# Kernel tuning notes

Hardware: AMD Instinct MI355X
Metric: run time of the kernel (lower is better)

The kernel has to match this reference:

```python
import jax, jax.numpy as jnp
import numpy as np

B, T, E, H, K, V = 64, 256, 300, 500, 64, 32000  # batch, seq, embed, hidden/dir, tags, vocab
PAD, EOS, SOS = 0, 1, 2
NEG = -10000.0


def setup_inputs() -> dict:
    key = jax.random.key(0)
    ks = jax.random.split(key, 20)
    rn = lambda k, shape, s=0.05: jax.random.normal(k, shape, jnp.float32) * s
    inp = {}
    inp["x"] = jax.random.randint(ks[0], (B, T), 3, V)   # all > 0 -> mask all ones (no padding)
    inp["y0"] = jax.random.randint(ks[1], (B, T), 3, K)  # gold tags, avoid PAD/EOS/SOS
    inp["embed"] = rn(ks[2], (V, E), 0.1)
    dims = [E, 2 * H]  # layer-0 input = embed, layer-1 input = concat(bi-dir hidden)
    i = 3
    for l in (0, 1):
        for d in ("f", "b"):
            inp[f"Wih{l}{d}"] = rn(ks[i], (4 * H, dims[l])); i += 1
            inp[f"Whh{l}{d}"] = rn(ks[i], (4 * H, H)); i += 1
            inp[f"b{l}{d}"] = rn(ks[i], (4 * H,)); i += 1
    inp["Wout"] = rn(ks[i], (K, 2 * H))
    inp["bout"] = rn(ks[i + 1], (K,))
    tr = jax.random.normal(ks[i + 2], (K, K), jnp.float32)
    tr = (tr.at[SOS, :].set(NEG).at[:, EOS].set(NEG).at[:, PAD].set(NEG)
            .at[PAD, :].set(NEG).at[PAD, EOS].set(0.0).at[PAD, PAD].set(0.0))
    inp["trans"] = tr  # trans[next, prev]
    return inp


def _lstm_dir(xs, Wih, Whh, b, reverse):
    """xs: [T,B,D] -> [T,B,H]; PyTorch gate order i,f,g,o."""
    if reverse:
        xs = xs[::-1]
    z0 = jnp.zeros((xs.shape[1], Whh.shape[1]), xs.dtype)

    def step(carry, xt):
        h, c = carry
        z = xt @ Wih.T + h @ Whh.T + b
        i_, f_, g_, o_ = jnp.split(z, 4, axis=-1)
        c = jax.nn.sigmoid(f_) * c + jax.nn.sigmoid(i_) * jnp.tanh(g_)
        h = jax.nn.sigmoid(o_) * jnp.tanh(c)
        return (h, c), h

    _, hs = jax.lax.scan(step, (z0, z0), xs)
    return hs[::-1] if reverse else hs


def reference(x, y0, embed, Wih0f, Whh0f, b0f, Wih0b, Whh0b, b0b,
              Wih1f, Whh1f, b1f, Wih1b, Whh1b, b1b, Wout, bout, trans):
    xs = embed[x].transpose(1, 0, 2)  # [T,B,E]
    h0 = jnp.concatenate([_lstm_dir(xs, Wih0f, Whh0f, b0f, False),
                          _lstm_dir(xs, Wih0b, Whh0b, b0b, True)], axis=-1)
    h1 = jnp.concatenate([_lstm_dir(h0, Wih1f, Whh1f, b1f, False),
                          _lstm_dir(h0, Wih1b, Whh1b, b1b, True)], axis=-1)
    emit = h1 @ Wout.T + bout                  # [T,B,K]
    mask = (x > 0).astype(emit.dtype).T        # [T,B]
    emit = emit * mask[..., None]              # y = y * mask

    # CRF partition (forward algorithm): new[b,j] = LSE_i(score[b,i] + trans[j,i]) + emit[t,b,j]
    init = jnp.full((B, K), NEG, emit.dtype).at[:, SOS].set(0.0)

    def step(score, em):
        e_t, m_t = em
        new = jax.nn.logsumexp(score[:, None, :] + trans[None, :, :], axis=-1) + e_t
        return jnp.where(m_t[:, None] > 0, new, score), None

    final, _ = jax.lax.scan(step, init, (emit, mask))
    Z = jax.nn.logsumexp(final, axis=-1)       # [B]

    # gold path score
    tags = jnp.concatenate([jnp.full((B, 1), SOS, y0.dtype), y0], axis=1)  # [B,T+1]
    e = jnp.take_along_axis(emit.transpose(1, 0, 2), tags[:, 1:, None], axis=2)[..., 0]  # [B,T]
    tr = trans[tags[:, 1:], tags[:, :-1]] * mask.T                                       # [B,T]
    gold = (e + tr).sum(axis=1)
    return Z - gold
```

## Files before the change

### kernel.cpp

```cpp
#include <hip/hip_runtime.h>
#include <hip/hip_bf16.h>

typedef short bf16x4 __attribute__((ext_vector_type(4)));
typedef short bf16x8 __attribute__((ext_vector_type(8)));
typedef short bf16x16 __attribute__((ext_vector_type(16)));
typedef float f32x4 __attribute__((ext_vector_type(4)));
typedef __hip_bfloat16 bf16;
typedef unsigned long long ull;

#define NEGV -10000.0f


__device__ __forceinline__ float sigm(float v) { return 1.0f / (1.0f + __expf(-v)); }
__device__ __forceinline__ float tanh_(float v) { float e = __expf(2.0f * v); return 1.0f - 2.0f / (e + 1.0f); }

__device__ __forceinline__ void async_load16(const bf16* g, const char* l) {
  __builtin_amdgcn_global_load_lds((const __attribute__((address_space(1))) void*)g,
                                   (__attribute__((address_space(3))) void*)l, 16, 0, 0);
}


__global__ __launch_bounds__(256) void pack_w0(const float* __restrict__ wf, const float* __restrict__ wb,
                                               bf16* __restrict__ dst) {
  int idx = blockIdx.x * 256 + threadIdx.x;
  int u = idx & 7, lane = (idx >> 3) & 63, rem = idx >> 9;
  int kt = rem % 10, nt = rem / 10;
  int n = (nt << 4) + (lane & 15), k = (kt << 5) + ((lane >> 4) << 3) + u;
  int d = n >> 11, g = (n >> 9) & 3, j = n & 511;
  float v = 0.f;
  if (j < 500 && k < 300) v = (d ? wb : wf)[(g * 500 + j) * 300 + k];
  dst[idx] = __float2bfloat16(v);
}

__global__ __launch_bounds__(256) void pack_whh(const float* __restrict__ w, bf16* __restrict__ dst) {
  int idx = blockIdx.x * 256 + threadIdx.x;
  int u = idx & 7, lane = (idx >> 3) & 63, rem = idx >> 9;
  int kt = rem & 15, nt = rem >> 4;
  int n = (nt << 4) + (lane & 15), k = (kt << 5) + ((lane >> 4) << 3) + u;
  int g = n >> 9, j = n & 511;
  float v = 0.f;
  if (j < 500 && k < 500) v = w[(g * 500 + j) * 500 + k];
  dst[idx] = __float2bfloat16(v);
}

__global__ __launch_bounds__(256) void pack_w1(const float* __restrict__ wf, const float* __restrict__ wb,
                                               bf16* __restrict__ dst) {
  int idx = blockIdx.x * 256 + threadIdx.x;
  int u = idx & 7, lane = (idx >> 3) & 63, rem = idx >> 9;
  int kt = rem & 31, nt = rem >> 5;
  int n = (nt << 4) + (lane & 15), k = (kt << 5) + ((lane >> 4) << 3) + u;
  int d = n >> 11, g = (n >> 9) & 3, j = n & 511;
  int kk = k & 511;
  int ks = (k < 512) ? kk : 500 + kk;
  float v = 0.f;
  if (j < 500 && kk < 500) v = (d ? wb : wf)[(g * 500 + j) * 1000 + ks];
  dst[idx] = __float2bfloat16(v);
}

__global__ __launch_bounds__(256) void pack_wout(const float* __restrict__ w, bf16* __restrict__ dst) {
  int idx = blockIdx.x * 256 + threadIdx.x;
  int u = idx & 7, lane = (idx >> 3) & 63, rem = idx >> 9;
  int kt = rem & 31, nt = rem >> 5;
  int n = (nt << 4) + (lane & 15), k = (kt << 5) + ((lane >> 4) << 3) + u;
  int kk = k & 511;
  int ks = (k < 512) ? kk : 500 + kk;
  float v = 0.f;
  if (kk < 500) v = w[n * 1000 + ks];
  dst[idx] = __float2bfloat16(v);
}

__global__ __launch_bounds__(256) void pack_bias(const float* __restrict__ bf_, const float* __restrict__ bb_,
                                                 float* __restrict__ dst) {
  int idx = blockIdx.x * 256 + threadIdx.x;
  int d = idx >> 11, g = (idx >> 9) & 3, j = idx & 511;
  dst[idx] = (j < 500) ? (d ? bb_ : bf_)[g * 500 + j] : 0.f;
}

__global__ __launch_bounds__(256) void embed_k(const int* __restrict__ x, const float* __restrict__ em,
                                               bf16* __restrict__ xs) {
  int idx = blockIdx.x * 256 + threadIdx.x;
  int e = idx % 320;
  int row = idx / 320;
  int t = row >> 6, b = row & 63;
  float v = 0.f;
  if (e < 300) {
    int xv = x[b * 256 + t];
    v = em[(size_t)xv * 300 + e];
  }
  xs[idx] = __float2bfloat16(v);
}

__global__ __launch_bounds__(256) void gemm_nt(const bf16* __restrict__ A, const bf16* __restrict__ Bf,
                                               bf16* __restrict__ C, int Kdim, int Kt) {
  const int lane = threadIdx.x & 63, wave = threadIdx.x >> 6;
  const int lr = lane & 15, lh = lane >> 4;
  const int mb = blockIdx.x * 64;
  const int ntb = blockIdx.y * 16 + wave * 4;
  f32x4 acc[4][4] = {};
  for (int kt = 0; kt < Kt; ++kt) {
    bf16x8 a[4], b[4];
#pragma unroll
    for (int mt = 0; mt < 4; ++mt)
      a[mt] = *(const bf16x8*)(A + (size_t)(mb + mt * 16 + lr) * Kdim + kt * 32 + lh * 8);
#pragma unroll
    for (int q = 0; q < 4; ++q)
      b[q] = *(const bf16x8*)(Bf + ((size_t)(ntb + q) * Kt + kt) * 512 + lane * 8);
#pragma unroll
    for (int mt = 0; mt < 4; ++mt)
#pragma unroll
      for (int q = 0; q < 4; ++q)
        acc[mt][q] = __builtin_amdgcn_mfma_f32_16x16x32_bf16(a[mt], b[q], acc[mt][q], 0, 0, 0);
  }
  const int t = blockIdx.x;
#pragma unroll
  for (int q = 0; q < 4; ++q) {
    const int colbase = (ntb + q) * 16;
    const int dirq = colbase >> 11, gq = (colbase >> 9) & 3, jbq = (colbase >> 4) & 31;
    unsigned short vals[16];
#pragma unroll
    for (int mt = 0; mt < 4; ++mt)
#pragma unroll
      for (int r = 0; r < 4; ++r) {
        bf16 hb = __float2bfloat16(acc[mt][q][r]);
        vals[mt * 4 + r] = *(unsigned short*)&hb;
      }
    bf16* outp = C + ((((size_t)t * 2 + dirq) * 32 + jbq) * 4 + gq) * 1024 + lane * 16;
    *(bf16x8*)(outp) = *(const bf16x8*)(vals);
    *(bf16x8*)(outp + 8) = *(const bf16x8*)(vals + 8);
  }
}

template <int ROWS>
__global__ __launch_bounds__(256, 1) void lstm_st(const bf16* __restrict__ preP, const bf16* __restrict__ whh,
                                                  const float* __restrict__ bias, bf16* __restrict__ hout,
                                                  unsigned int* __restrict__ flags) {
  constexpr int MT = ROWS / 16;
  constexpr int NPART = 64 / ROWS;
  const int tid = threadIdx.x, lane = tid & 63, wave = tid >> 6;
  const int lr = lane & 15, lh = lane >> 4;
  const int jb = blockIdx.x, dir = blockIdx.y, part = blockIdx.z;
  unsigned int* flg = flags + (dir * NPART + part) * 64;
  unsigned int* myflg = flg + jb;
  __shared__ __align__(64) char hlds[ROWS * 1040];
  __shared__ float xch[4 * ROWS * 17];
  __shared__ float cst[ROWS * 16];
  for (int i = tid; i < ROWS * 16; i += 256) cst[i] = 0.f;
  const float bb = bias[dir * 2048 + wave * 512 + jb * 16 + lr];
  const bf16* wbase = whh + ((size_t)(dir * 128 + wave * 32 + jb) * 16) * 512 + lane * 8;

  bf16x8 wfrag[16];
#pragma unroll
  for (int kt = 0; kt < 16; ++kt) wfrag[kt] = *(const bf16x8*)(wbase + kt * 512);

  unsigned short pf[MT * 4];
  {
    const int t0 = dir ? 255 : 0;
    const bf16* pb = preP + ((((size_t)t0 * 2 + dir) * 32 + jb) * 4 + wave) * 1024 + lane * 16 + part * MT * 4;
    if constexpr (MT == 1) *(bf16x4*)pf = *(const bf16x4*)pb;
    else if constexpr (MT == 2) *(bf16x8*)pf = *(const bf16x8*)pb;
    else *(bf16x16*)pf = *(const bf16x16*)pb;
  }

  for (int s = 0; s < 256; ++s) {
    const int t = dir ? 255 - s : s;
    f32x4 acc[MT] = {};
    if (s > 0) {
      const unsigned int tgt = (unsigned int)s;
      for (;;) {
        unsigned int v = __hip_atomic_load(flg + (lane & 31), __ATOMIC_RELAXED, __HIP_MEMORY_SCOPE_AGENT);
        if (__all((int)(v >= tgt))) break;
      }
      asm volatile("" ::: "memory");
      const int tp = dir ? t + 1 : t - 1;
      const bf16* hp = hout + (size_t)tp * 65536 + dir * 512;
#pragma unroll
      for (int i = 0; i < ROWS / 4; ++i) {
        const int row = i * 4 + wave;
        async_load16(hp + (size_t)(part * ROWS + row) * 1024 + lane * 8, hlds + row * 1040);
      }
      asm volatile("s_waitcnt vmcnt(0)" ::: "memory");
      __syncthreads();
#pragma unroll 4
      for (int kt = 0; kt < 16; ++kt) {
#pragma unroll
        for (int mt = 0; mt < MT; ++mt) {
          const int row = mt * 16 + lr;
          const bf16x8 afr = *(const bf16x8*)(hlds + row * 1040 + kt * 64 + lh * 16);
          acc[mt] = __builtin_amdgcn_mfma_f32_16x16x32_bf16(afr, wfrag[kt], acc[mt], 0, 0, 0);
        }
      }
    }
#pragma unroll
    for (int mt = 0; mt < MT; ++mt)
#pragma unroll
      for (int r = 0; r < 4; ++r) {
        bf16 pv; *(unsigned short*)&pv = pf[mt * 4 + r];
        xch[(wave * ROWS + mt * 16 + lh * 4 + r) * 17 + lr] = acc[mt][r] + bb + __bfloat162float(pv);
      }
    __syncthreads();
    if (tid < ROWS * 8) {
      const int row = tid >> 3, c0 = (tid & 7) * 2;
      unsigned int pk = 0;
#pragma unroll
      for (int i = 0; i < 2; ++i) {
        int col = c0 + i;
        float gi = xch[(0 * ROWS + row) * 17 + col];
        float gf = xch[(1 * ROWS + row) * 17 + col];
        float gg = xch[(2 * ROWS + row) * 17 + col];
        float go = xch[(3 * ROWS + row) * 17 + col];
        float c = cst[row * 16 + col];
        float cn = sigm(gf) * c + sigm(gi) * tanh_(gg);
        cst[row * 16 + col] = cn;
        bf16 hb = __float2bfloat16(sigm(go) * tanh_(cn));
        pk |= (unsigned int)(*(unsigned short*)&hb) << (16 * i);
      }
      unsigned int* hq =
          (unsigned int*)(hout + ((size_t)t * 64 + part * ROWS + row) * 1024 + dir * 512 + jb * 16 + c0);
      __hip_atomic_store(hq, pk, __ATOMIC_RELAXED, __HIP_MEMORY_SCOPE_AGENT);
    }
    asm volatile("s_waitcnt vmcnt(0)" ::: "memory");
    __syncthreads();
    if (tid == 0)
      __hip_atomic_store(myflg, (unsigned int)(s + 1), __ATOMIC_RELAXED, __HIP_MEMORY_SCOPE_AGENT);
    if (s < 255) {
      const int tn = dir ? t - 1 : t + 1;
      const bf16* pb = preP + ((((size_t)tn * 2 + dir) * 32 + jb) * 4 + wave) * 1024 + lane * 16 + part * MT * 4;
      if constexpr (MT == 1) *(bf16x4*)pf = *(const bf16x4*)pb;
      else if constexpr (MT == 2) *(bf16x8*)pf = *(const bf16x8*)pb;
      else *(bf16x16*)pf = *(const bf16x16*)pb;
    }
  }
}

__global__ __launch_bounds__(256) void emit_k(const bf16* __restrict__ h1, const bf16* __restrict__ wo,
                                              const float* __restrict__ bout, const int* __restrict__ x,
                                              float* __restrict__ emit) {
  const int tid = threadIdx.x, lane = tid & 63, wave = tid >> 6;
  const int lr = lane & 15, lh = lane >> 4;
  const int mb = blockIdx.x * 64 + wave * 16;
  f32x4 acc[4] = {};
  for (int kt = 0; kt < 32; ++kt) {
    bf16x8 a = *(const bf16x8*)(h1 + (size_t)(mb + lr) * 1024 + kt * 32 + lh * 8);
#pragma unroll
    for (int q = 0; q < 4; ++q) {
      bf16x8 b = *(const bf16x8*)(wo + ((size_t)(q * 32 + kt) * 64 + lane) * 8);
      acc[q] = __builtin_amdgcn_mfma_f32_16x16x32_bf16(a, b, acc[q], 0, 0, 0);
    }
  }
#pragma unroll
  for (int q = 0; q < 4; ++q)
#pragma unroll
    for (int r = 0; r < 4; ++r) {
      int row = mb + lh * 4 + r;
      int col = q * 16 + lr;
      int tt = row >> 6, bi = row & 63;
      float m = (x[bi * 256 + tt] > 0) ? 1.f : 0.f;
      emit[(size_t)row * 64 + col] = (acc[q][r] + bout[col]) * m;
    }
}

__global__ __launch_bounds__(256) void crf_k(const float* __restrict__ emit, const float* __restrict__ trans,
                                             const int* __restrict__ x, const int* __restrict__ y0,
                                             float* __restrict__ out) {
  const int b = blockIdx.x, tid = threadIdx.x;
  __shared__ float tr[4096];
  __shared__ float sc[2][64];
  __shared__ float pm[4][64], ps[4][64];
  __shared__ float redw[4];
  for (int i = tid; i < 4096; i += 256) tr[i] = trans[i];
  if (tid < 64) sc[0][tid] = (tid == 2) ? 0.f : NEGV;
  __syncthreads();
  {
    const int t = tid;
    const int tag = y0[b * 256 + t];
    const int prev = t ? y0[b * 256 + t - 1] : 2;
    const float m = (x[b * 256 + t] > 0) ? 1.f : 0.f;
    float g = emit[((size_t)t * 64 + b) * 64 + tag] + tr[tag * 64 + prev] * m;
    for (int o = 32; o; o >>= 1) g += __shfl_down(g, o, 64);
    if ((tid & 63) == 0) redw[tid >> 6] = g;
  }
  __syncthreads();
  const float gold = redw[0] + redw[1] + redw[2] + redw[3];
  const int j = tid & 63, kq = tid >> 6;
  int cur = 0;
  for (int t = 0; t < 256; ++t) {
    const float* trj = tr + j * 64 + kq * 16;
    const float* scc = sc[cur] + kq * 16;
    float v[16];
    float mx = -3.0e38f;
#pragma unroll
    for (int k = 0; k < 16; ++k) {
      v[k] = scc[k] + trj[k];
      mx = fmaxf(mx, v[k]);
    }
    float sm = 0.f;
#pragma unroll
    for (int k = 0; k < 16; ++k) sm += __expf(v[k] - mx);
    pm[kq][j] = mx;
    ps[kq][j] = sm;
    __syncthreads();
    if (kq == 0) {
      float M = fmaxf(fmaxf(pm[0][j], pm[1][j]), fmaxf(pm[2][j], pm[3][j]));
      float S = ps[0][j] * __expf(pm[0][j] - M) + ps[1][j] * __expf(pm[1][j] - M) +
                ps[2][j] * __expf(pm[2][j] - M) + ps[3][j] * __expf(pm[3][j] - M);
      float nv = M + __logf(S) + emit[((size_t)t * 64 + b) * 64 + j];
      sc[cur ^ 1][j] = (x[b * 256 + t] > 0) ? nv : sc[cur][j];
    }
    __syncthreads();
    cur ^= 1;
  }
  if (tid < 64) {
    float v2 = sc[cur][tid];
    float M = v2;
    for (int o = 32; o; o >>= 1) M = fmaxf(M, __shfl_xor(M, o, 64));
    float s2 = __expf(v2 - M);
    for (int o = 32; o; o >>= 1) s2 += __shfl_xor(s2, o, 64);
    if (tid == 0) out[b] = M + __logf(s2) - gold;
  }
}

extern "C" void kernel_launch(void* const* d_in, const int* in_sizes, int n_in, void* d_out, int out_size,
                              void* d_ws, size_t ws_size, hipStream_t stream) {
  (void)in_sizes; (void)n_in; (void)out_size; (void)ws_size;
  const int* x = (const int*)d_in[0];
  const int* y0 = (const int*)d_in[1];
  const float* embed = (const float*)d_in[2];
  const float* Wih0f = (const float*)d_in[3];
  const float* Whh0f = (const float*)d_in[4];
  const float* b0f = (const float*)d_in[5];
  const float* Wih0b = (const float*)d_in[6];
  const float* Whh0b = (const float*)d_in[7];
  const float* b0b = (const float*)d_in[8];
  const float* Wih1f = (const float*)d_in[9];
  const float* Whh1f = (const float*)d_in[10];
  const float* b1f = (const float*)d_in[11];
  const float* Wih1b = (const float*)d_in[12];
  const float* Whh1b = (const float*)d_in[13];
  const float* b1b = (const float*)d_in[14];
  const float* Wout = (const float*)d_in[15];
  const float* bout = (const float*)d_in[16];
  const float* trans = (const float*)d_in[17];

  char* p = (char*)d_ws;
  auto take = [&](size_t n) { char* r = p; p += (n + 255) & ~(size_t)255; return r; };
  unsigned int* flags = (unsigned int*)take(2048 * sizeof(unsigned int));
  bf16* xs = (bf16*)take(16384ull * 320 * 2);
  bf16* preP = (bf16*)take(16384ull * 4096 * 2);
  bf16* h0 = (bf16*)take(16384ull * 1024 * 2);
  bf16* h1 = (bf16*)take(16384ull * 1024 * 2);
  float* emitb = (float*)take(16384ull * 64 * 4);
  bf16* W0B = (bf16*)take(4096ull * 320 * 2);
  bf16* W1B = (bf16*)take(4096ull * 1024 * 2);
  bf16* WhhB = (bf16*)take(4ull * 1048576 * 2);
  bf16* WoB = (bf16*)take(64ull * 1024 * 2);
  float* bias0 = (float*)take(4096 * 4);
  float* bias1 = (float*)take(4096 * 4);

  hipMemsetAsync(flags, 0, 2048 * sizeof(unsigned int), stream);
  hipLaunchKernelGGL(pack_w0, dim3(5120), dim3(256), 0, stream, Wih0f, Wih0b, W0B);
  hipLaunchKernelGGL(pack_whh, dim3(4096), dim3(256), 0, stream, Whh0f, WhhB + 0ull * 1048576);
  hipLaunchKernelGGL(pack_whh, dim3(4096), dim3(256), 0, stream, Whh0b, WhhB + 1ull * 1048576);
  hipLaunchKernelGGL(pack_whh, dim3(4096), dim3(256), 0, stream, Whh1f, WhhB + 2ull * 1048576);
  hipLaunchKernelGGL(pack_whh, dim3(4096), dim3(256), 0, stream, Whh1b, WhhB + 3ull * 1048576);
  hipLaunchKernelGGL(pack_w1, dim3(16384), dim3(256), 0, stream, Wih1f, Wih1b, W1B);
  hipLaunchKernelGGL(pack_wout, dim3(256), dim3(256), 0, stream, Wout, WoB);
  hipLaunchKernelGGL(pack_bias, dim3(16), dim3(256), 0, stream, b0f, b0b, bias0);
  hipLaunchKernelGGL(pack_bias, dim3(16), dim3(256), 0, stream, b1f, b1b, bias1);
  hipLaunchKernelGGL(embed_k, dim3(20480), dim3(256), 0, stream, x, embed, xs);

  hipLaunchKernelGGL(gemm_nt, dim3(256, 16), dim3(256), 0, stream, xs, W0B, preP, 320, 10);
  {
    const bf16* a0 = preP; const bf16* a1 = WhhB; const float* a2 = bias0; bf16* a3 = h0;
    unsigned int* a4 = flags;
    void* args[] = {&a0, &a1, &a2, &a3, &a4};
    hipLaunchCooperativeKernel((void*)(&lstm_st<16>), dim3(32, 2, 4), dim3(256), args, 0, stream);
  }
  hipLaunchKernelGGL(gemm_nt, dim3(256, 16), dim3(256), 0, stream, h0, W1B, preP, 1024, 32);
  {
    const bf16* a0 = preP; const bf16* a1 = WhhB + 2ull * 1048576; const float* a2 = bias1; bf16* a3 = h1;
    unsigned int* a4 = flags + 1024;
    void* args[] = {&a0, &a1, &a2, &a3, &a4};
    hipLaunchCooperativeKernel((void*)(&lstm_st<32>), dim3(32, 2, 2), dim3(256), args, 0, stream);
  }
  hipLaunchKernelGGL(emit_k, dim3(256), dim3(256), 0, stream, h1, WoB, bout, x, emitb);
  hipLaunchKernelGGL(crf_k, dim3(64), dim3(256), 0, stream, emitb, trans, x, y0, (float*)d_out);
}
```

Before: 3.118 ms.

## Add LDS-resident weight variant for layer-0 LSTM and merge pack kernels

Layer 0's recurrent kernel now uses 32 rows per block (128 blocks instead of 256). Its recurrent weights are held in shared memory instead of registers, and the previous hidden state is read straight from global memory into the matrix-multiply operands, with no LDS staging or barrier. Layer 1 keeps the old register-weight path. The gate exchange buffer is padded to a stride of 18 so float2 reads are possible, and the four Whh packing launches and two bias packing launches are each merged into one. The aim is fewer per-step barriers and less cross-block flag traffic in layer 0, at the cost of 64KB of LDS per block and global loads of h on the critical path of every step.

```diff
diff --git a/kernel.cpp b/kernel.cpp
--- a/kernel.cpp
+++ b/kernel.cpp
@@ -1,7 +1,6 @@
 #include <hip/hip_runtime.h>
 #include <hip/hip_bf16.h>
 
-typedef short bf16x4 __attribute__((ext_vector_type(4)));
 typedef short bf16x8 __attribute__((ext_vector_type(8)));
 typedef short bf16x16 __attribute__((ext_vector_type(16)));
 typedef float f32x4 __attribute__((ext_vector_type(4)));
@@ -32,7 +31,11 @@
   dst[idx] = __float2bfloat16(v);
 }
 
-__global__ __launch_bounds__(256) void pack_whh(const float* __restrict__ w, bf16* __restrict__ dst) {
+__global__ __launch_bounds__(256) void pack_whh4(const float* __restrict__ w0f, const float* __restrict__ w0b,
+                                                 const float* __restrict__ w1f, const float* __restrict__ w1b,
+                                                 bf16* __restrict__ dst) {
+  const int which = blockIdx.y;
+  const float* w = which == 0 ? w0f : which == 1 ? w0b : which == 2 ? w1f : w1b;
   int idx = blockIdx.x * 256 + threadIdx.x;
   int u = idx & 7, lane = (idx >> 3) & 63, rem = idx >> 9;
   int kt = rem & 15, nt = rem >> 4;
@@ -40,7 +43,7 @@
   int g = n >> 9, j = n & 511;
   float v = 0.f;
   if (j < 500 && k < 500) v = w[(g * 500 + j) * 500 + k];
-  dst[idx] = __float2bfloat16(v);
+  dst[(size_t)which * 1048576 + idx] = __float2bfloat16(v);
 }
 
 __global__ __launch_bounds__(256) void pack_w1(const float* __restrict__ wf, const float* __restrict__ wb,
@@ -69,11 +72,15 @@
   dst[idx] = __float2bfloat16(v);
 }
 
-__global__ __launch_bounds__(256) void pack_bias(const float* __restrict__ bf_, const float* __restrict__ bb_,
-                                                 float* __restrict__ dst) {
-  int idx = blockIdx.x * 256 + threadIdx.x;
-  int d = idx >> 11, g = (idx >> 9) & 3, j = idx & 511;
-  dst[idx] = (j < 500) ? (d ? bb_ : bf_)[g * 500 + j] : 0.f;
+__global__ __launch_bounds__(256) void pack_bias2(const float* __restrict__ b0f, const float* __restrict__ b0b,
+                                                  const float* __restrict__ b1f, const float* __restrict__ b1b,
+                                                  float* __restrict__ dst0, float* __restrict__ dst1) {
+  int idx = blockIdx.x * 256 + threadIdx.x;
+  int layer = idx >> 12, w = idx & 4095;
+  int d = w >> 11, g = (w >> 9) & 3, j = w & 511;
+  const float* src = layer ? (d ? b1b : b1f) : (d ? b0b : b0f);
+  float v = (j < 500) ? src[g * 500 + j] : 0.f;
+  (layer ? dst1 : dst0)[w] = v;
 }
 
 __global__ __launch_bounds__(256) void embed_k(const int* __restrict__ x, const float* __restrict__ em,
@@ -130,35 +137,40 @@
   }
 }
 
-template <int ROWS>
+template <int STAGE>
 __global__ __launch_bounds__(256, 1) void lstm_st(const bf16* __restrict__ preP, const bf16* __restrict__ whh,
                                                   const float* __restrict__ bias, bf16* __restrict__ hout,
                                                   unsigned int* __restrict__ flags) {
-  constexpr int MT = ROWS / 16;
-  constexpr int NPART = 64 / ROWS;
+  constexpr int ROWS = 32, MT = 2;
   const int tid = threadIdx.x, lane = tid & 63, wave = tid >> 6;
   const int lr = lane & 15, lh = lane >> 4;
   const int jb = blockIdx.x, dir = blockIdx.y, part = blockIdx.z;
-  unsigned int* flg = flags + (dir * NPART + part) * 64;
+  unsigned int* flg = flags + (dir * 2 + part) * 64;
   unsigned int* myflg = flg + jb;
-  __shared__ __align__(64) char hlds[ROWS * 1040];
-  __shared__ float xch[4 * ROWS * 17];
+  __shared__ __align__(64) char wh_or_h[STAGE ? ROWS * 1040 : 65536];
+  __shared__ float xch[4 * ROWS * 18];
   __shared__ float cst[ROWS * 16];
   for (int i = tid; i < ROWS * 16; i += 256) cst[i] = 0.f;
   const float bb = bias[dir * 2048 + wave * 512 + jb * 16 + lr];
-  const bf16* wbase = whh + ((size_t)(dir * 128 + wave * 32 + jb) * 16) * 512 + lane * 8;
-
-  bf16x8 wfrag[16];
-#pragma unroll
-  for (int kt = 0; kt < 16; ++kt) wfrag[kt] = *(const bf16x8*)(wbase + kt * 512);
-
-  unsigned short pf[MT * 4];
+  const bf16* wbase = whh + ((size_t)(dir * 128 + wave * 32 + jb) * 16) * 512;
+
+  bf16x8 wfrag[STAGE ? 16 : 1];
+  if (STAGE) {
+#pragma unroll
+    for (int kt = 0; kt < 16; ++kt) wfrag[kt] = *(const bf16x8*)(wbase + kt * 512 + lane * 8);
+  } else {
+#pragma unroll
+    for (int kt = 0; kt < 16; ++kt)
+      async_load16(wbase + kt * 512 + lane * 8, wh_or_h + (wave * 16 + kt) * 1024 + lane * 16);
+    asm volatile("s_waitcnt vmcnt(0)" ::: "memory");
+    __syncthreads();
+  }
+
+  unsigned short pf[8];
   {
     const int t0 = dir ? 255 : 0;
-    const bf16* pb = preP + ((((size_t)t0 * 2 + dir) * 32 + jb) * 4 + wave) * 1024 + lane * 16 + part * MT * 4;
-    if constexpr (MT == 1) *(bf16x4*)pf = *(const bf16x4*)pb;
-    else if constexpr (MT == 2) *(bf16x8*)pf = *(const bf16x8*)pb;
-    else *(bf16x16*)pf = *(const bf16x16*)pb;
+    *(bf16x8*)pf = *(const bf16x8*)(preP + ((((size_t)t0 * 2 + dir) * 32 + jb) * 4 + wave) * 1024 +
+                                    lane * 16 + part * 8);
   }
 
   for (int s = 0; s < 256; ++s) {
@@ -172,21 +184,34 @@
       }
       asm volatile("" ::: "memory");
       const int tp = dir ? t + 1 : t - 1;
-      const bf16* hp = hout + (size_t)tp * 65536 + dir * 512;
-#pragma unroll
-      for (int i = 0; i < ROWS / 4; ++i) {
-        const int row = i * 4 + wave;
-        async_load16(hp + (size_t)(part * ROWS + row) * 1024 + lane * 8, hlds + row * 1040);
-      }
-      asm volatile("s_waitcnt vmcnt(0)" ::: "memory");
-      __syncthreads();
+      if (STAGE) {
+        const bf16* hp = hout + (size_t)tp * 65536 + dir * 512;
+#pragma unroll
+        for (int i = 0; i < ROWS / 4; ++i) {
+          const int row = i * 4 + wave;
+          async_load16(hp + (size_t)(part * ROWS + row) * 1024 + lane * 8, wh_or_h + row * 1040);
+        }
+        asm volatile("s_waitcnt vmcnt(0)" ::: "memory");
+        __syncthreads();
 #pragma unroll 4
-      for (int kt = 0; kt < 16; ++kt) {
-#pragma unroll
-        for (int mt = 0; mt < MT; ++mt) {
-          const int row = mt * 16 + lr;
-          const bf16x8 afr = *(const bf16x8*)(hlds + row * 1040 + kt * 64 + lh * 16);
-          acc[mt] = __builtin_amdgcn_mfma_f32_16x16x32_bf16(afr, wfrag[kt], acc[mt], 0, 0, 0);
+        for (int kt = 0; kt < 16; ++kt) {
+#pragma unroll
+          for (int mt = 0; mt < MT; ++mt) {
+            const int row = mt * 16 + lr;
+            const bf16x8 afr = *(const bf16x8*)(wh_or_h + row * 1040 + kt * 64 + lh * 16);
+            acc[mt] = __builtin_amdgcn_mfma_f32_16x16x32_bf16(afr, wfrag[kt], acc[mt], 0, 0, 0);
+          }
+        }
+      } else {
+        const bf16* hp = hout + (size_t)tp * 65536 + dir * 512 +
+                         (size_t)(part * ROWS + lr) * 1024 + lh * 8;
+#pragma unroll 4
+        for (int kt = 0; kt < 16; ++kt) {
+          bf16x8 wf = *(const bf16x8*)(wh_or_h + (wave * 16 + kt) * 1024 + lane * 16);
+          bf16x8 a0 = *(const bf16x8*)(hp + kt * 32);
+          bf16x8 a1 = *(const bf16x8*)(hp + 16384 + kt * 32);
+          acc[0] = __builtin_amdgcn_mfma_f32_16x16x32_bf16(a0, wf, acc[0], 0, 0, 0);
+          acc[1] = __builtin_amdgcn_mfma_f32_16x16x32_bf16(a1, wf, acc[1], 0, 0, 0);
         }
       }
     }
@@ -195,23 +220,24 @@
 #pragma unroll
       for (int r = 0; r < 4; ++r) {
         bf16 pv; *(unsigned short*)&pv = pf[mt * 4 + r];
-        xch[(wave * ROWS + mt * 16 + lh * 4 + r) * 17 + lr] = acc[mt][r] + bb + __bfloat162float(pv);
+        xch[(wave * ROWS + mt * 16 + lh * 4 + r) * 18 + lr] = acc[mt][r] + bb + __bfloat162float(pv);
       }
     __syncthreads();
-    if (tid < ROWS * 8) {
+    {
       const int row = tid >> 3, c0 = (tid & 7) * 2;
       unsigned int pk = 0;
+      float2 gi = *(const float2*)&xch[(0 * ROWS + row) * 18 + c0];
+      float2 gf = *(const float2*)&xch[(1 * ROWS + row) * 18 + c0];
+      float2 gg = *(const float2*)&xch[(2 * ROWS + row) * 18 + c0];
+      float2 go = *(const float2*)&xch[(3 * ROWS + row) * 18 + c0];
 #pragma unroll
       for (int i = 0; i < 2; ++i) {
-        int col = c0 + i;
-        float gi = xch[(0 * ROWS + row) * 17 + col];
-        float gf = xch[(1 * ROWS + row) * 17 + col];
-        float gg = xch[(2 * ROWS + row) * 17 + col];
-        float go = xch[(3 * ROWS + row) * 17 + col];
-        float c = cst[row * 16 + col];
-        float cn = sigm(gf) * c + sigm(gi) * tanh_(gg);
-        cst[row * 16 + col] = cn;
-        bf16 hb = __float2bfloat16(sigm(go) * tanh_(cn));
+        float giv = i ? gi.y : gi.x, gfv = i ? gf.y : gf.x;
+        float ggv = i ? gg.y : gg.x, gov = i ? go.y : go.x;
+        float c = cst[row * 16 + c0 + i];
+        float cn = sigm(gfv) * c + sigm(giv) * tanh_(ggv);
+        cst[row * 16 + c0 + i] = cn;
+        bf16 hb = __float2bfloat16(sigm(gov) * tanh_(cn));
         pk |= (unsigned int)(*(unsigned short*)&hb) << (16 * i);
       }
       unsigned int* hq =
@@ -224,10 +250,8 @@
       __hip_atomic_store(myflg, (unsigned int)(s + 1), __ATOMIC_RELAXED, __HIP_MEMORY_SCOPE_AGENT);
     if (s < 255) {
       const int tn = dir ? t - 1 : t + 1;
-      const bf16* pb = preP + ((((size_t)tn * 2 + dir) * 32 + jb) * 4 + wave) * 1024 + lane * 16 + part * MT * 4;
-      if constexpr (MT == 1) *(bf16x4*)pf = *(const bf16x4*)pb;
-      else if constexpr (MT == 2) *(bf16x8*)pf = *(const bf16x8*)pb;
-      else *(bf16x16*)pf = *(const bf16x16*)pb;
+      *(bf16x8*)pf = *(const bf16x8*)(preP + ((((size_t)tn * 2 + dir) * 32 + jb) * 4 + wave) * 1024 +
+                                      lane * 16 + part * 8);
     }
   }
 }
@@ -358,14 +382,10 @@
 
   hipMemsetAsync(flags, 0, 2048 * sizeof(unsigned int), stream);
   hipLaunchKernelGGL(pack_w0, dim3(5120), dim3(256), 0, stream, Wih0f, Wih0b, W0B);
-  hipLaunchKernelGGL(pack_whh, dim3(4096), dim3(256), 0, stream, Whh0f, WhhB + 0ull * 1048576);
-  hipLaunchKernelGGL(pack_whh, dim3(4096), dim3(256), 0, stream, Whh0b, WhhB + 1ull * 1048576);
-  hipLaunchKernelGGL(pack_whh, dim3(4096), dim3(256), 0, stream, Whh1f, WhhB + 2ull * 1048576);
-  hipLaunchKernelGGL(pack_whh, dim3(4096), dim3(256), 0, stream, Whh1b, WhhB + 3ull * 1048576);
+  hipLaunchKernelGGL(pack_whh4, dim3(4096, 4), dim3(256), 0, stream, Whh0f, Whh0b, Whh1f, Whh1b, WhhB);
   hipLaunchKernelGGL(pack_w1, dim3(16384), dim3(256), 0, stream, Wih1f, Wih1b, W1B);
   hipLaunchKernelGGL(pack_wout, dim3(256), dim3(256), 0, stream, Wout, WoB);
-  hipLaunchKernelGGL(pack_bias, dim3(16), dim3(256), 0, stream, b0f, b0b, bias0);
-  hipLaunchKernelGGL(pack_bias, dim3(16), dim3(256), 0, stream, b1f, b1b, bias1);
+  hipLaunchKernelGGL(pack_bias2, dim3(32), dim3(256), 0, stream, b0f, b0b, b1f, b1b, bias0, bias1);
   hipLaunchKernelGGL(embed_k, dim3(20480), dim3(256), 0, stream, x, embed, xs);
 
   hipLaunchKernelGGL(gemm_nt, dim3(256, 16), dim3(256), 0, stream, xs, W0B, preP, 320, 10);
@@ -373,14 +393,14 @@
     const bf16* a0 = preP; const bf16* a1 = WhhB; const float* a2 = bias0; bf16* a3 = h0;
     unsigned int* a4 = flags;
     void* args[] = {&a0, &a1, &a2, &a3, &a4};
-    hipLaunchCooperativeKernel((void*)(&lstm_st<16>), dim3(32, 2, 4), dim3(256), args, 0, stream);
+    hipLaunchCooperativeKernel((void*)(&lstm_st<0>), dim3(32, 2, 2), dim3(256), args, 0, stream);
   }
   hipLaunchKernelGGL(gemm_nt, dim3(256, 16), dim3(256), 0, stream, h0, W1B, preP, 1024, 32);
   {
     const bf16* a0 = preP; const bf16* a1 = WhhB + 2ull * 1048576; const float* a2 = bias1; bf16* a3 = h1;
     unsigned int* a4 = flags + 1024;
     void* args[] = {&a0, &a1, &a2, &a3, &a4};
-    hipLaunchCooperativeKernel((void*)(&lstm_st<32>), dim3(32, 2, 2), dim3(256), args, 0, stream);
+    hipLaunchCooperativeKernel((void*)(&lstm_st<1>), dim3(32, 2, 2), dim3(256), args, 0, stream);
   }
   hipLaunchKernelGGL(emit_k, dim3(256), dim3(256), 0, stream, h1, WoB, bout, x, emitb);
   hipLaunchKernelGGL(crf_k, dim3(64), dim3(256), 0, stream, emitb, trans, x, y0, (float*)d_out);
```

Result: slower. 3.647 ms (+17.0%).
